# Performance work log

Measured on AMD Instinct MI355X. Metric: run time of the kernel, lower is better.

Reference implementation:

```python
import jax, jax.numpy as jnp
import numpy as np

N_NODES = 100000
N_EDGES = 1600000
DIM_IN = 128
DIM_OUT = 128


def setup_inputs() -> dict:
    key = jax.random.key(0)
    k1, k2, k3, k4, k5 = jax.random.split(key, 5)
    x = jax.random.normal(k1, (N_NODES, DIM_IN), dtype=jnp.float32)
    # Dense kernel (glorot-style scale)
    W = jax.random.normal(k2, (DIM_IN, DIM_OUT), dtype=jnp.float32) * (1.0 / np.sqrt(DIM_IN))
    edge_vals = jax.random.uniform(k3, (N_EDGES,), dtype=jnp.float32)
    edge_rows = jax.random.randint(k4, (N_EDGES,), 0, N_NODES, dtype=jnp.int32)
    edge_cols = jax.random.randint(k5, (N_EDGES,), 0, N_NODES, dtype=jnp.int32)
    return {"x": x, "W": W, "edge_vals": edge_vals,
            "edge_rows": edge_rows, "edge_cols": edge_cols}


def reference(x, W, edge_vals, edge_rows, edge_cols):
    # Dense projection (Dense, use_bias=False): [N, dim_in] @ [dim_in, dim_out]
    h = x @ W
    # Sparse adjacency SpMM in COO form:
    # out[r] = sum_{edges e with row r} vals[e] * h[col[e]]
    msgs = edge_vals[:, None] * h[edge_cols]            # [E, dim_out]
    out = jax.ops.segment_sum(msgs, edge_rows, num_segments=N_NODES)
    return out
```

## Files before the change

### kernel.cpp

```cpp
#include <hip/hip_runtime.h>
#include <hip/hip_bf16.h>
#include <hip/hip_fp16.h>


#define DIM 128
#define RB 128
#define NB_MAX 1024
#define CH 4096
#define REG_CAP 2560

typedef short s16x8 __attribute__((ext_vector_type(8)));
typedef float f32x4 __attribute__((ext_vector_type(4)));
typedef unsigned short u16;
typedef unsigned long long u64;
typedef u16 u16x4 __attribute__((ext_vector_type(4)));
typedef u16 u16x8 __attribute__((ext_vector_type(8)));

static __device__ __forceinline__ u16 f2bf(float f) {
  union { float f; unsigned u; } a; a.f = f;
  return (u16)((a.u + 0x7fffu + ((a.u >> 16) & 1u)) >> 16);
}
static __device__ __forceinline__ float bf_lo(unsigned u) {
  union { unsigned u; float f; } a; a.u = u << 16; return a.f;
}
static __device__ __forceinline__ float bf_hi(unsigned u) {
  union { unsigned u; float f; } a; a.u = u & 0xffff0000u; return a.f;
}
static __device__ __forceinline__ u16 f2h(float f) {
  return __half_as_ushort(__float2half(f));
}
static __device__ __forceinline__ float h2f(u16 h) {
  return __half2float(__ushort_as_half(h));
}

__global__ __launch_bounds__(256) void repack_w_kernel(
    const float* __restrict__ W, u16* __restrict__ Wp) {
  int e = blockIdx.x * 256 + threadIdx.x;
  int k = e >> 7, n = e & 127;
  Wp[((k >> 3) * 128 + n) * 8 + (k & 7)] = f2bf(W[e]);
}

static __device__ __forceinline__ void gemm_body(
    const float* __restrict__ x, const u16* __restrict__ Wp,
    u16* __restrict__ hb, int n_nodes, int m0, u16* xl) {
  const int t = threadIdx.x;

  const float4* x4 = (const float4*)x;
#pragma unroll
  for (int it = 0; it < 16; ++it) {
    int i = it * 256 + t;
    int r = i >> 5, c = i & 31;
    float4 v = make_float4(0.f, 0.f, 0.f, 0.f);
    int node = m0 + r;
    if (node < n_nodes) v = x4[(size_t)node * 32 + c];
    u16x4 pk = {f2bf(v.x), f2bf(v.y), f2bf(v.z), f2bf(v.w)};
    *(u16x4*)&xl[r * 136 + c * 4] = pk;
  }
  __syncthreads();

  const int w = t >> 6, l = t & 63, q = l >> 4, n15 = l & 15;

  f32x4 acc[2][8];
#pragma unroll
  for (int mt = 0; mt < 2; ++mt)
#pragma unroll
    for (int nt = 0; nt < 8; ++nt) acc[mt][nt] = (f32x4){0.f, 0.f, 0.f, 0.f};

#pragma unroll
  for (int ks = 0; ks < 4; ++ks) {
    s16x8 a0 = *(const s16x8*)&xl[(w * 32 + n15) * 136 + ks * 32 + q * 8];
    s16x8 a1 = *(const s16x8*)&xl[(w * 32 + 16 + n15) * 136 + ks * 32 + q * 8];
#pragma unroll
    for (int nt = 0; nt < 8; ++nt) {
      s16x8 b = *(const s16x8*)&Wp[(size_t)(((ks * 4 + q) * 128) + nt * 16 + n15) * 8];
      acc[0][nt] = __builtin_amdgcn_mfma_f32_16x16x32_bf16(a0, b, acc[0][nt], 0, 0, 0);
      acc[1][nt] = __builtin_amdgcn_mfma_f32_16x16x32_bf16(a1, b, acc[1][nt], 0, 0, 0);
    }
  }
  __syncthreads();

#pragma unroll
  for (int mt = 0; mt < 2; ++mt)
#pragma unroll
    for (int nt = 0; nt < 8; ++nt)
#pragma unroll
      for (int r_ = 0; r_ < 4; ++r_)
        xl[(w * 32 + mt * 16 + q * 4 + r_) * 136 + nt * 16 + n15] =
            f2bf(acc[mt][nt][r_]);
  __syncthreads();

#pragma unroll
  for (int it = 0; it < 8; ++it) {
    int chunk = it * 256 + t;
    int r = chunk >> 4, c = chunk & 15;
    int node = m0 + r;
    if (node < n_nodes)
      *(u16x8*)(hb + (size_t)node * 128 + c * 8) = *(const u16x8*)&xl[r * 136 + c * 8];
  }
}

static __device__ __forceinline__ void part_body(
    const int* __restrict__ rows, const int* __restrict__ cols,
    const float* __restrict__ vals, int* __restrict__ gcur,
    u64* __restrict__ reg, int n_edges, int nb, int base,
    int* hist, int* ofs, int* gbase, int* lcur, int* tsum, u64* srec) {
  const int t = threadIdx.x;

  for (int i = t; i < NB_MAX; i += 256) { hist[i] = 0; lcur[i] = 0; }
  __syncthreads();

  int r[16], c[16];
  float v[16];
  bool ok[16];
#pragma unroll
  for (int i = 0; i < 16; ++i) {
    int e = base + i * 256 + t;
    ok[i] = e < n_edges;
    r[i] = ok[i] ? rows[e] : 0;
    c[i] = ok[i] ? cols[e] : 0;
    v[i] = ok[i] ? vals[e] : 0.f;
    if (ok[i]) atomicAdd(&hist[r[i] >> 7], 1);
  }
  __syncthreads();

  const int b0 = t * 4;
  int h0 = hist[b0], h1 = hist[b0 + 1], h2 = hist[b0 + 2], h3 = hist[b0 + 3];
  int run = h0 + h1 + h2 + h3;
  tsum[t] = run;
  for (int b = t; b < nb; b += 256) {
    int hc = hist[b];
    gbase[b] = (hc > 0) ? atomicAdd(&gcur[b], hc) : 0;
  }
  __syncthreads();
  for (int off = 1; off < 256; off <<= 1) {
    int x2 = (t >= off) ? tsum[t - off] : 0;
    __syncthreads();
    tsum[t] += x2;
    __syncthreads();
  }
  int ex = tsum[t] - run;
  ofs[b0] = ex;
  ofs[b0 + 1] = ex + h0;
  ofs[b0 + 2] = ex + h0 + h1;
  ofs[b0 + 3] = ex + h0 + h1 + h2;
  __syncthreads();

#pragma unroll
  for (int i = 0; i < 16; ++i) {
    if (ok[i]) {
      int bkt = r[i] >> 7;
      int pos = ofs[bkt] + atomicAdd(&lcur[bkt], 1);
      srec[pos] = ((u64)(unsigned)r[i] << 33) | ((u64)(unsigned)c[i] << 16) |
                  (u64)f2h(v[i]);
    }
  }
  __syncthreads();

  int nvalid = n_edges - base;
  if (nvalid > CH) nvalid = CH;
  for (int i = t; i < nvalid; i += 256) {
    u64 rec = srec[i];
    int row = (int)(rec >> 33);
    int bkt = row >> 7;
    int dst = gbase[bkt] + (i - ofs[bkt]);
    if (dst < REG_CAP) reg[(size_t)bkt * REG_CAP + dst] = rec;
  }
}

__global__ __launch_bounds__(256) void gemm_part_kernel(
    const float* __restrict__ x, const u16* __restrict__ Wp, u16* __restrict__ hb,
    const int* __restrict__ rows, const int* __restrict__ cols,
    const float* __restrict__ vals, int* __restrict__ gcur, u64* __restrict__ reg,
    int n_nodes, int n_edges, int nb, int gA, int gP) {
  __shared__ union {
    u16 xl[128 * 136];
    struct {
      int hist[NB_MAX];
      int ofs[NB_MAX];
      int gbase[NB_MAX];
      int lcur[NB_MAX];
      int tsum[256];
      u64 srec[CH];
    } p;
  } sh;

  int bid = blockIdx.x;
  bool isP;
  int id;
  if (gA == 2 * gP) {
    int r = bid % 3, q = bid / 3;
    isP = (r == 2);
    id = isP ? q : q * 2 + r;
  } else {
    isP = bid < gP;
    id = isP ? bid : bid - gP;
  }

  if (!isP) {
    gemm_body(x, Wp, hb, n_nodes, id * 128, sh.xl);
  } else {
    part_body(rows, cols, vals, gcur, reg, n_edges, nb, id * CH,
              sh.p.hist, sh.p.ofs, sh.p.gbase, sh.p.lcur, sh.p.tsum, sh.p.srec);
  }
}

__global__ __launch_bounds__(256) void mfma_gemm_kernel(
    const float* __restrict__ x, const u16* __restrict__ Wp,
    u16* __restrict__ hb, int n_nodes) {
  __shared__ u16 xl[128 * 136];
  gemm_body(x, Wp, hb, n_nodes, blockIdx.x * 128, xl);
}

__global__ __launch_bounds__(1024, 6) void bucket_accum_kernel(
    const u16* __restrict__ hb, const u64* __restrict__ reg,
    const int* __restrict__ gcur, float* __restrict__ out, int n_nodes) {
  __shared__ int hist[RB];
  __shared__ int ofs[RB];
  __shared__ int lcur[RB];
  __shared__ u64 srt[REG_CAP];

  const int t = threadIdx.x;
  const int b = blockIdx.x;
  const int row0 = b * RB;

  int n_e = gcur[b];
  if (n_e > REG_CAP) n_e = REG_CAP;

  if (t < RB) { hist[t] = 0; lcur[t] = 0; }
  __syncthreads();

  u64 rr[3];
  int rl[3];
  bool ok[3];
#pragma unroll
  for (int i = 0; i < 3; ++i) {
    int j = i * 1024 + t;
    ok[i] = j < n_e;
    rr[i] = ok[i] ? reg[(size_t)b * REG_CAP + j] : 0;
    rl[i] = (int)(rr[i] >> 33) & (RB - 1);
    if (ok[i]) atomicAdd(&hist[rl[i]], 1);
  }
  __syncthreads();

  if (t < 64) {
    int h0 = hist[2 * t], h1 = hist[2 * t + 1];
    int s = h0 + h1;
    int v = s;
#pragma unroll
    for (int off = 1; off < 64; off <<= 1) {
      int u = __shfl_up(v, off, 64);
      if (t >= off) v += u;
    }
    int ex = v - s;
    ofs[2 * t] = ex;
    ofs[2 * t + 1] = ex + h0;
  }
  __syncthreads();

#pragma unroll
  for (int i = 0; i < 3; ++i) {
    if (ok[i]) {
      int pos = ofs[rl[i]] + atomicAdd(&lcur[rl[i]], 1);
      srt[pos] = rr[i];
    }
  }
  __syncthreads();

  const int lane = t & 63;
  const int w = t >> 6;
  const int q = lane >> 4;
  const int li = lane & 15;
  const int r0 = w * 8 + q * 2;

  const uint4* h4 = (const uint4*)hb;
  float4* out4 = (float4*)out;

#pragma unroll
  for (int k = 0; k < 2; ++k) {
    int rli = r0 + k;
    int gr = row0 + rli;
    if (gr < n_nodes && hist[rli] == 0) {
      out4[(size_t)gr * 32 + li * 2] = make_float4(0.f, 0.f, 0.f, 0.f);
      out4[(size_t)gr * 32 + li * 2 + 1] = make_float4(0.f, 0.f, 0.f, 0.f);
    }
  }

  int qs0 = ofs[r0];
  int qs1 = ofs[r0 + 1] + hist[r0 + 1];

  if (qs1 > qs0) {
    float a0 = 0.f, a1 = 0.f, a2 = 0.f, a3 = 0.f;
    float a4 = 0.f, a5 = 0.f, a6 = 0.f, a7 = 0.f;
    int cur = (int)(srt[qs0] >> 33) & (RB - 1);

    for (int p = qs0; p < qs1; p += 4) {
      uint4 uu[4];
      unsigned mv[4];
#pragma unroll
      for (int j = 0; j < 4; ++j) {
        int idx = p + j;
        idx = idx < qs1 ? idx : qs1 - 1;
        u64 rec = srt[idx];
        int col = (int)((rec >> 16) & 0x1FFFF);
        mv[j] = ((unsigned)((rec >> 33) & (RB - 1)) << 16) | (unsigned)(rec & 0xFFFF);
        uu[j] = h4[(size_t)col * 16 + li];
      }
#pragma unroll
      for (int j = 0; j < 4; ++j) {
        if (p + j < qs1) {
          int lr = (int)(mv[j] >> 16);
          if (lr != cur) {
            size_t o = (size_t)(row0 + cur) * 32 + li * 2;
            out4[o] = make_float4(a0, a1, a2, a3);
            out4[o + 1] = make_float4(a4, a5, a6, a7);
            a0 = a1 = a2 = a3 = a4 = a5 = a6 = a7 = 0.f;
            cur = lr;
          }
          float vv = h2f((u16)(mv[j] & 0xFFFF));
          a0 += vv * bf_lo(uu[j].x);
          a1 += vv * bf_hi(uu[j].x);
          a2 += vv * bf_lo(uu[j].y);
          a3 += vv * bf_hi(uu[j].y);
          a4 += vv * bf_lo(uu[j].z);
          a5 += vv * bf_hi(uu[j].z);
          a6 += vv * bf_lo(uu[j].w);
          a7 += vv * bf_hi(uu[j].w);
        }
      }
    }
    size_t o = (size_t)(row0 + cur) * 32 + li * 2;
    out4[o] = make_float4(a0, a1, a2, a3);
    out4[o + 1] = make_float4(a4, a5, a6, a7);
  }
}

__global__ __launch_bounds__(256) void scatter_kernel(
    const u16* __restrict__ hb, const float* __restrict__ vals,
    const int* __restrict__ rows, const int* __restrict__ cols,
    float* __restrict__ out, int n_edges) {
  const int lane = threadIdx.x & 63;
  const int wid = (blockIdx.x * blockDim.x + threadIdx.x) >> 6;
  const int nwaves = (gridDim.x * blockDim.x) >> 6;
  const unsigned* h32 = (const unsigned*)hb;
  for (int e = wid; e < n_edges; e += nwaves) {
    int r = rows[e];
    int c = cols[e];
    float v = vals[e];
    unsigned u = h32[(size_t)c * 64 + lane];
    float* op = out + (size_t)r * DIM + 2 * lane;
    atomicAdd(op, v * bf_lo(u));
    atomicAdd(op + 1, v * bf_hi(u));
  }
}

extern "C" void kernel_launch(void* const* d_in, const int* in_sizes, int n_in,
                              void* d_out, int out_size, void* d_ws, size_t ws_size,
                              hipStream_t stream) {
  const float* x = (const float*)d_in[0];
  const float* W = (const float*)d_in[1];
  const float* edge_vals = (const float*)d_in[2];
  const int* edge_rows = (const int*)d_in[3];
  const int* edge_cols = (const int*)d_in[4];
  float* out = (float*)d_out;

  const int n_nodes = in_sizes[0] / DIM;
  const int n_edges = in_sizes[2];
  const int nb = (n_nodes + RB - 1) / RB;

  char* p = (char*)d_ws;
  u16* hb = (u16*)p;   p += (((size_t)n_nodes * DIM * 2 + 15) / 16) * 16;
  u16* Wp = (u16*)p;   p += (size_t)DIM * DIM * 2;
  int* gcur = (int*)p; p += (((size_t)nb * 4 + 15) / 16) * 16;
  u64* reg = (u64*)p;  p += (size_t)nb * REG_CAP * 8;
  const size_t need = (size_t)(p - (char*)d_ws);

  repack_w_kernel<<<64, 256, 0, stream>>>(W, Wp);

  if (ws_size < need || nb > NB_MAX) {
    mfma_gemm_kernel<<<(n_nodes + 127) / 128, 256, 0, stream>>>(x, Wp, hb, n_nodes);
    hipMemsetAsync(d_out, 0, (size_t)out_size * sizeof(float), stream);
    scatter_kernel<<<2048, 256, 0, stream>>>(hb, edge_vals, edge_rows, edge_cols,
                                             out, n_edges);
    return;
  }

  hipMemsetAsync(gcur, 0, (size_t)nb * sizeof(int), stream);

  const int gA = (n_nodes + 127) / 128;
  const int gP = (n_edges + CH - 1) / CH;
  gemm_part_kernel<<<gA + gP, 256, 0, stream>>>(x, Wp, hb, edge_rows, edge_cols,
                                                edge_vals, gcur, reg, n_nodes,
                                                n_edges, nb, gA, gP);

  bucket_accum_kernel<<<nb, 1024, 0, stream>>>(hb, reg, gcur, out, n_nodes);
}
```

Measured before the change: 223.9 us.

## Use wave-shuffle scan in partition and persistent grid-stride bucket accumulation

The partition block's 256-thread shared-memory Hillis-Steele scan becomes a wavefront shuffle scan plus a small per-wave sum combine, dropping many block barriers. The bucket accumulation kernel becomes persistent: a capped grid of 512 blocks loops over buckets. It raises the occupancy hint from 6 to 8 and widens the gather prefetch depth from 4 to 6 rows. This trades more live registers and a trailing barrier per bucket for fewer launches and barriers and more loads in flight.

```diff
diff --git a/kernel.cpp b/kernel.cpp
--- a/kernel.cpp
+++ b/kernel.cpp
@@ -8,6 +8,8 @@
 #define NB_MAX 1024
 #define CH 4096
 #define REG_CAP 2560
+#define P2_GRID 512
+#define DEPTH 6
 
 typedef short s16x8 __attribute__((ext_vector_type(8)));
 typedef float f32x4 __attribute__((ext_vector_type(4)));
@@ -103,8 +105,10 @@
     const int* __restrict__ rows, const int* __restrict__ cols,
     const float* __restrict__ vals, int* __restrict__ gcur,
     u64* __restrict__ reg, int n_edges, int nb, int base,
-    int* hist, int* ofs, int* gbase, int* lcur, int* tsum, u64* srec) {
+    int* hist, int* ofs, int* gbase, int* lcur, int* wsum, u64* srec) {
   const int t = threadIdx.x;
+  const int lane = t & 63;
+  const int wid = t >> 6;
 
   for (int i = t; i < NB_MAX; i += 256) { hist[i] = 0; lcur[i] = 0; }
   __syncthreads();
@@ -126,19 +130,25 @@
   const int b0 = t * 4;
   int h0 = hist[b0], h1 = hist[b0 + 1], h2 = hist[b0 + 2], h3 = hist[b0 + 3];
   int run = h0 + h1 + h2 + h3;
-  tsum[t] = run;
+
   for (int b = t; b < nb; b += 256) {
     int hc = hist[b];
     gbase[b] = (hc > 0) ? atomicAdd(&gcur[b], hc) : 0;
   }
-  __syncthreads();
-  for (int off = 1; off < 256; off <<= 1) {
-    int x2 = (t >= off) ? tsum[t - off] : 0;
-    __syncthreads();
-    tsum[t] += x2;
-    __syncthreads();
-  }
-  int ex = tsum[t] - run;
+
+  int vsc = run;
+#pragma unroll
+  for (int off = 1; off < 64; off <<= 1) {
+    int u = __shfl_up(vsc, off, 64);
+    if (lane >= off) vsc += u;
+  }
+  if (lane == 63) wsum[wid] = vsc;
+  __syncthreads();
+  int wbase = 0;
+#pragma unroll
+  for (int ww = 0; ww < 3; ++ww)
+    if (ww < wid) wbase += wsum[ww];
+  int ex = wbase + vsc - run;
   ofs[b0] = ex;
   ofs[b0 + 1] = ex + h0;
   ofs[b0 + 2] = ex + h0 + h1;
@@ -179,7 +189,7 @@
       int ofs[NB_MAX];
       int gbase[NB_MAX];
       int lcur[NB_MAX];
-      int tsum[256];
+      int wsum[4];
       u64 srec[CH];
     } p;
   } sh;
@@ -200,7 +210,7 @@
     gemm_body(x, Wp, hb, n_nodes, id * 128, sh.xl);
   } else {
     part_body(rows, cols, vals, gcur, reg, n_edges, nb, id * CH,
-              sh.p.hist, sh.p.ofs, sh.p.gbase, sh.p.lcur, sh.p.tsum, sh.p.srec);
+              sh.p.hist, sh.p.ofs, sh.p.gbase, sh.p.lcur, sh.p.wsum, sh.p.srec);
   }
 }
 
@@ -211,61 +221,15 @@
   gemm_body(x, Wp, hb, n_nodes, blockIdx.x * 128, xl);
 }
 
-__global__ __launch_bounds__(1024, 6) void bucket_accum_kernel(
+__global__ __launch_bounds__(1024, 8) void bucket_accum_kernel(
     const u16* __restrict__ hb, const u64* __restrict__ reg,
-    const int* __restrict__ gcur, float* __restrict__ out, int n_nodes) {
+    const int* __restrict__ gcur, float* __restrict__ out, int n_nodes, int nb) {
   __shared__ int hist[RB];
   __shared__ int ofs[RB];
   __shared__ int lcur[RB];
   __shared__ u64 srt[REG_CAP];
 
   const int t = threadIdx.x;
-  const int b = blockIdx.x;
-  const int row0 = b * RB;
-
-  int n_e = gcur[b];
-  if (n_e > REG_CAP) n_e = REG_CAP;
-
-  if (t < RB) { hist[t] = 0; lcur[t] = 0; }
-  __syncthreads();
-
-  u64 rr[3];
-  int rl[3];
-  bool ok[3];
-#pragma unroll
-  for (int i = 0; i < 3; ++i) {
-    int j = i * 1024 + t;
-    ok[i] = j < n_e;
-    rr[i] = ok[i] ? reg[(size_t)b * REG_CAP + j] : 0;
-    rl[i] = (int)(rr[i] >> 33) & (RB - 1);
-    if (ok[i]) atomicAdd(&hist[rl[i]], 1);
-  }
-  __syncthreads();
-
-  if (t < 64) {
-    int h0 = hist[2 * t], h1 = hist[2 * t + 1];
-    int s = h0 + h1;
-    int v = s;
-#pragma unroll
-    for (int off = 1; off < 64; off <<= 1) {
-      int u = __shfl_up(v, off, 64);
-      if (t >= off) v += u;
-    }
-    int ex = v - s;
-    ofs[2 * t] = ex;
-    ofs[2 * t + 1] = ex + h0;
-  }
-  __syncthreads();
-
-#pragma unroll
-  for (int i = 0; i < 3; ++i) {
-    if (ok[i]) {
-      int pos = ofs[rl[i]] + atomicAdd(&lcur[rl[i]], 1);
-      srt[pos] = rr[i];
-    }
-  }
-  __syncthreads();
-
   const int lane = t & 63;
   const int w = t >> 6;
   const int q = lane >> 4;
@@ -275,62 +239,111 @@
   const uint4* h4 = (const uint4*)hb;
   float4* out4 = (float4*)out;
 
-#pragma unroll
-  for (int k = 0; k < 2; ++k) {
-    int rli = r0 + k;
-    int gr = row0 + rli;
-    if (gr < n_nodes && hist[rli] == 0) {
-      out4[(size_t)gr * 32 + li * 2] = make_float4(0.f, 0.f, 0.f, 0.f);
-      out4[(size_t)gr * 32 + li * 2 + 1] = make_float4(0.f, 0.f, 0.f, 0.f);
-    }
-  }
-
-  int qs0 = ofs[r0];
-  int qs1 = ofs[r0 + 1] + hist[r0 + 1];
-
-  if (qs1 > qs0) {
-    float a0 = 0.f, a1 = 0.f, a2 = 0.f, a3 = 0.f;
-    float a4 = 0.f, a5 = 0.f, a6 = 0.f, a7 = 0.f;
-    int cur = (int)(srt[qs0] >> 33) & (RB - 1);
-
-    for (int p = qs0; p < qs1; p += 4) {
-      uint4 uu[4];
-      unsigned mv[4];
-#pragma unroll
-      for (int j = 0; j < 4; ++j) {
-        int idx = p + j;
-        idx = idx < qs1 ? idx : qs1 - 1;
-        u64 rec = srt[idx];
-        int col = (int)((rec >> 16) & 0x1FFFF);
-        mv[j] = ((unsigned)((rec >> 33) & (RB - 1)) << 16) | (unsigned)(rec & 0xFFFF);
-        uu[j] = h4[(size_t)col * 16 + li];
+  for (int b = blockIdx.x; b < nb; b += gridDim.x) {
+    const int row0 = b * RB;
+
+    int n_e = gcur[b];
+    if (n_e > REG_CAP) n_e = REG_CAP;
+
+    if (t < RB) { hist[t] = 0; lcur[t] = 0; }
+    __syncthreads();
+
+    u64 rr[3];
+    int rl[3];
+    bool ok[3];
+#pragma unroll
+    for (int i = 0; i < 3; ++i) {
+      int j = i * 1024 + t;
+      ok[i] = j < n_e;
+      rr[i] = ok[i] ? reg[(size_t)b * REG_CAP + j] : 0;
+      rl[i] = (int)(rr[i] >> 33) & (RB - 1);
+      if (ok[i]) atomicAdd(&hist[rl[i]], 1);
+    }
+    __syncthreads();
+
+    if (t < 64) {
+      int h0 = hist[2 * t], h1 = hist[2 * t + 1];
+      int s = h0 + h1;
+      int v = s;
+#pragma unroll
+      for (int off = 1; off < 64; off <<= 1) {
+        int u = __shfl_up(v, off, 64);
+        if (t >= off) v += u;
       }
-#pragma unroll
-      for (int j = 0; j < 4; ++j) {
-        if (p + j < qs1) {
-          int lr = (int)(mv[j] >> 16);
-          if (lr != cur) {
-            size_t o = (size_t)(row0 + cur) * 32 + li * 2;
-            out4[o] = make_float4(a0, a1, a2, a3);
-            out4[o + 1] = make_float4(a4, a5, a6, a7);
-            a0 = a1 = a2 = a3 = a4 = a5 = a6 = a7 = 0.f;
-            cur = lr;
+      int ex = v - s;
+      ofs[2 * t] = ex;
+      ofs[2 * t + 1] = ex + h0;
+    }
+    __syncthreads();
+
+#pragma unroll
+    for (int i = 0; i < 3; ++i) {
+      if (ok[i]) {
+        int pos = ofs[rl[i]] + atomicAdd(&lcur[rl[i]], 1);
+        srt[pos] = rr[i];
+      }
+    }
+    __syncthreads();
+
+#pragma unroll
+    for (int k = 0; k < 2; ++k) {
+      int rli = r0 + k;
+      int gr = row0 + rli;
+      if (gr < n_nodes && hist[rli] == 0) {
+        out4[(size_t)gr * 32 + li * 2] = make_float4(0.f, 0.f, 0.f, 0.f);
+        out4[(size_t)gr * 32 + li * 2 + 1] = make_float4(0.f, 0.f, 0.f, 0.f);
+      }
+    }
+
+    int qs0 = ofs[r0];
+    int qs1 = ofs[r0 + 1] + hist[r0 + 1];
+
+    if (qs1 > qs0) {
+      float a0 = 0.f, a1 = 0.f, a2 = 0.f, a3 = 0.f;
+      float a4 = 0.f, a5 = 0.f, a6 = 0.f, a7 = 0.f;
+      int cur = (int)(srt[qs0] >> 33) & (RB - 1);
+
+      for (int p = qs0; p < qs1; p += DEPTH) {
+        uint4 uu[DEPTH];
+        unsigned mv[DEPTH];
+#pragma unroll
+        for (int j = 0; j < DEPTH; ++j) {
+          int idx = p + j;
+          idx = idx < qs1 ? idx : qs1 - 1;
+          u64 rec = srt[idx];
+          int col = (int)((rec >> 16) & 0x1FFFF);
+          mv[j] = ((unsigned)((rec >> 33) & (RB - 1)) << 16) | (unsigned)(rec & 0xFFFF);
+          uu[j] = h4[(size_t)col * 16 + li];
+        }
+#pragma unroll
+        for (int j = 0; j < DEPTH; ++j) {
+          if (p + j < qs1) {
+            int lr = (int)(mv[j] >> 16);
+            if (lr != cur) {
+              size_t o = (size_t)(row0 + cur) * 32 + li * 2;
+              out4[o] = make_float4(a0, a1, a2, a3);
+              out4[o + 1] = make_float4(a4, a5, a6, a7);
+              a0 = a1 = a2 = a3 = a4 = a5 = a6 = a7 = 0.f;
+              cur = lr;
+            }
+            float vv = h2f((u16)(mv[j] & 0xFFFF));
+            a0 += vv * bf_lo(uu[j].x);
+            a1 += vv * bf_hi(uu[j].x);
+            a2 += vv * bf_lo(uu[j].y);
+            a3 += vv * bf_hi(uu[j].y);
+            a4 += vv * bf_lo(uu[j].z);
+            a5 += vv * bf_hi(uu[j].z);
+            a6 += vv * bf_lo(uu[j].w);
+            a7 += vv * bf_hi(uu[j].w);
           }
-          float vv = h2f((u16)(mv[j] & 0xFFFF));
-          a0 += vv * bf_lo(uu[j].x);
-          a1 += vv * bf_hi(uu[j].x);
-          a2 += vv * bf_lo(uu[j].y);
-          a3 += vv * bf_hi(uu[j].y);
-          a4 += vv * bf_lo(uu[j].z);
-          a5 += vv * bf_hi(uu[j].z);
-          a6 += vv * bf_lo(uu[j].w);
-          a7 += vv * bf_hi(uu[j].w);
         }
       }
-    }
-    size_t o = (size_t)(row0 + cur) * 32 + li * 2;
-    out4[o] = make_float4(a0, a1, a2, a3);
-    out4[o + 1] = make_float4(a4, a5, a6, a7);
+      size_t o = (size_t)(row0 + cur) * 32 + li * 2;
+      out4[o] = make_float4(a0, a1, a2, a3);
+      out4[o + 1] = make_float4(a4, a5, a6, a7);
+    }
+
+    __syncthreads();
   }
 }
 
@@ -392,5 +405,7 @@
                                                 edge_vals, gcur, reg, n_nodes,
                                                 n_edges, nb, gA, gP);
 
-  bucket_accum_kernel<<<nb, 1024, 0, stream>>>(hb, reg, gcur, out, n_nodes);
-}
+  int p2_grid = nb < P2_GRID ? nb : P2_GRID;
+  bucket_accum_kernel<<<p2_grid, 1024, 0, stream>>>(hb, reg, gcur, out,
+                                                    n_nodes, nb);
+}
```

Result: slower. 232.7 us (+3.9%).
